# Optimization experiments

Hardware: AMD Instinct MI355X
Metric: run time of the kernel (lower is better)

Reference implementation:

```python
import jax, jax.numpy as jnp
import numpy as np

NUM_HEADS = 16
D_MODEL = 1024
D_K = D_MODEL // NUM_HEADS


def setup_inputs() -> dict:
    key = jax.random.key(0)
    ks = jax.random.split(key, 11)
    B, S, D = 1, 4096, D_MODEL
    scale = 1.0 / np.sqrt(D)
    return {
        "Q": jax.random.normal(ks[0], (B, S, D), jnp.float32),
        "K": jax.random.normal(ks[1], (B, S, D), jnp.float32),
        "V": jax.random.normal(ks[2], (B, S, D), jnp.float32),
        "W_Q": jax.random.normal(ks[3], (D, D), jnp.float32) * scale,
        "b_Q": jax.random.normal(ks[4], (D,), jnp.float32) * 0.02,
        "W_K": jax.random.normal(ks[5], (D, D), jnp.float32) * scale,
        "b_K": jax.random.normal(ks[6], (D,), jnp.float32) * 0.02,
        "W_V": jax.random.normal(ks[7], (D, D), jnp.float32) * scale,
        "b_V": jax.random.normal(ks[8], (D,), jnp.float32) * 0.02,
        "W_O": jax.random.normal(ks[9], (D, D), jnp.float32) * scale,
        "b_O": jax.random.normal(ks[10], (D,), jnp.float32) * 0.02,
    }


def _split_heads(x):
    # (B, S, D) -> (B, H, S, d_k)
    B, S, _ = x.shape
    return x.reshape(B, S, NUM_HEADS, D_K).transpose(0, 2, 1, 3)


def reference(Q, K, V, W_Q, b_Q, W_K, b_K, W_V, b_V, W_O, b_O):
    q = _split_heads(Q @ W_Q + b_Q)  # (B, H, S, d_k)
    k = _split_heads(K @ W_K + b_K)
    v = _split_heads(V @ W_V + b_V)
    inv_sqrt_dk = jnp.asarray(1.0 / np.sqrt(D_K), q.dtype)
    scores = jnp.einsum("bhqd,bhkd->bhqk", q, k) * inv_sqrt_dk  # (B, H, S, S)
    weights = jax.nn.softmax(scores, axis=-1)
    out = jnp.einsum("bhqk,bhkd->bhqd", weights, v)  # (B, H, S, d_k)
    B, _, S, _ = out.shape
    combined = out.transpose(0, 2, 1, 3).reshape(B, S, D_MODEL)
    return combined @ W_O + b_O
```

## Files before the change

kernel.cpp:

```cpp
#include <hip/hip_runtime.h>

typedef float f32x2 __attribute__((ext_vector_type(2)));
typedef float f32x4 __attribute__((ext_vector_type(4)));
typedef float f32x16 __attribute__((ext_vector_type(16)));
typedef short bf16x8 __attribute__((ext_vector_type(8)));
typedef unsigned u32x2 __attribute__((ext_vector_type(2)));
typedef unsigned short u16;

#define S_LEN 4096
#define DMODEL 1024
#define NH 16
#define DK 64

#define SCALE_Q 0.18033688f

static __device__ __forceinline__ u16 f2bf(float x) {
  union { float f; unsigned u; } v; v.f = x;
  unsigned r = v.u + 0x7fffu + ((v.u >> 16) & 1u);
  return (u16)(r >> 16);
}

static __device__ __forceinline__ float bf2f(u16 x) {
  union { unsigned u; float f; } v; v.u = ((unsigned)x) << 16;
  return v.f;
}

#if __has_builtin(__builtin_amdgcn_exp2f)
#define EXP2F __builtin_amdgcn_exp2f
#else
#define EXP2F exp2f
#endif

static __device__ __forceinline__ unsigned pkbf(float lo, float hi) {
  unsigned r;
  asm("v_cvt_pk_bf16_f32 %0, %1, %2" : "=v"(r) : "v"(lo), "v"(hi));
  return r;
}

static __device__ __forceinline__ void plswap(unsigned& a, unsigned& b, int hi) {
#if __has_builtin(__builtin_amdgcn_permlane32_swap)
  u32x2 r = __builtin_amdgcn_permlane32_swap(a, b, false, false);
  a = r.x; b = r.y;
  (void)hi;
#else
  unsigned ax = __shfl_xor(a, 32), bx = __shfl_xor(b, 32);
  unsigned na = hi ? bx : a;
  unsigned nb = hi ? b : ax;
  a = na; b = nb;
#endif
}

static __device__ __forceinline__ void gload16(const void* g, void* l) {
  void* gg = (void*)g;
  __builtin_amdgcn_global_load_lds(
      (__attribute__((address_space(1))) void*)gg,
      (__attribute__((address_space(3))) void*)l, 16, 0, 0);
}

__global__ __launch_bounds__(256) void wcast4(const float* __restrict__ W0,
                                              const float* __restrict__ W1,
                                              const float* __restrict__ W2,
                                              const float* __restrict__ W3,
                                              u16* __restrict__ Wt) {
  __shared__ float t[32][33];
  const int z = blockIdx.z;
  const float* W = (z == 0) ? W0 : (z == 1) ? W1 : (z == 2) ? W2 : W3;
  u16* dst = Wt + (size_t)z * DMODEL * DMODEL;
  const int x = threadIdx.x, y = threadIdx.y;
  const int n0 = blockIdx.x * 32, k0 = blockIdx.y * 32;
#pragma unroll
  for (int i = 0; i < 4; ++i)
    t[y + 8 * i][x] = W[(size_t)(k0 + y + 8 * i) * DMODEL + n0 + x];
  __syncthreads();
#pragma unroll
  for (int i = 0; i < 4; ++i)
    dst[(size_t)(n0 + y + 8 * i) * DMODEL + k0 + x] = f2bf(t[x][y + 8 * i]);
}

__global__ __launch_bounds__(256) void castbf3(const float* __restrict__ A,
                                               const float* __restrict__ B,
                                               const float* __restrict__ C,
                                               u16* __restrict__ out) {
  const int z = blockIdx.x >> 10;
  const int b = blockIdx.x & 1023;
  const float* src = (z == 0) ? A : (z == 1) ? B : C;
  u16* dst = out + (size_t)z * S_LEN * DMODEL;
  const int n8 = S_LEN * DMODEL / 8;
  for (int i = b * 256 + threadIdx.x; i < n8; i += 1024 * 256) {
    float4 a = ((const float4*)src)[2 * i];
    float4 c = ((const float4*)src)[2 * i + 1];
    union { ushort4 u[2]; int4 q; } t;
    t.u[0].x = f2bf(a.x); t.u[0].y = f2bf(a.y);
    t.u[0].z = f2bf(a.z); t.u[0].w = f2bf(a.w);
    t.u[1].x = f2bf(c.x); t.u[1].y = f2bf(c.y);
    t.u[1].z = f2bf(c.z); t.u[1].w = f2bf(c.w);
    ((int4*)dst)[i] = t.q;
  }
}

template <int MODE>
__global__ __launch_bounds__(256) void pgemm(const u16* __restrict__ Abase,
                                             const u16* __restrict__ Btbase,
                                             const float* __restrict__ bq,
                                             const float* __restrict__ bk,
                                             const float* __restrict__ bv,
                                             void* __restrict__ outbase) {
  __shared__ __align__(16) char Al[16384];
  __shared__ __align__(16) char Bl[16384];
  const int nblk = gridDim.x, cpx = nblk >> 3;
  const int b0 = blockIdx.x;
  const int bid = (b0 & 7) * cpx + (b0 >> 3);
  const int z = (MODE == 0) ? (bid >> 8) : 0;
  const int rem = bid & 255;
  const int nb = rem & 7, mb = rem >> 3;
  const int m0 = mb * 128, n0 = nb * 128;
  const int tid = threadIdx.x, lane = tid & 63, wid = tid >> 6;
  const int gq = lane >> 4, c16 = lane & 15;
  const int wm = (wid >> 1) * 64, wn = (wid & 1) * 64;
  const char* Ab = (const char*)(Abase + (size_t)z * S_LEN * DMODEL);
  const char* Bb = (const char*)(Btbase + (size_t)z * DMODEL * DMODEL);
  const float* bias = (z == 0) ? bq : (z == 1 ? bk : bv);
  const float scale = (MODE == 0 && z == 0) ? SCALE_Q : 1.0f;

  f32x4 acc[4][4] = {};

  for (int kt = 0; kt < 16; ++kt) {
    const int kb = kt * 128;
#pragma unroll
    for (int p = 0; p < 4; ++p) {
      int lin = p * 4096 + tid * 16;
      int row = lin >> 7;
      int colg = (lin & 127) ^ ((row & 7) << 4);
      gload16(Ab + (size_t)(m0 + row) * 2048 + kb + colg,
              Al + p * 4096 + wid * 1024);
    }
#pragma unroll
    for (int p = 0; p < 4; ++p) {
      int lin = p * 4096 + tid * 16;
      int row = lin >> 7;
      int colg = (lin & 127) ^ ((row & 7) << 4);
      gload16(Bb + (size_t)(n0 + row) * 2048 + kb + colg,
              Bl + p * 4096 + wid * 1024);
    }
    __syncthreads();
#pragma unroll
    for (int kk = 0; kk < 2; ++kk) {
      bf16x8 a[4], b[4];
#pragma unroll
      for (int m = 0; m < 4; ++m) {
        int row = wm + m * 16 + c16;
        a[m] = *(const bf16x8*)(Al + row * 128 +
                                ((kk * 64 + gq * 16) ^ ((row & 7) << 4)));
      }
#pragma unroll
      for (int n = 0; n < 4; ++n) {
        int row = wn + n * 16 + c16;
        b[n] = *(const bf16x8*)(Bl + row * 128 +
                                ((kk * 64 + gq * 16) ^ ((row & 7) << 4)));
      }
#pragma unroll
      for (int m = 0; m < 4; ++m)
#pragma unroll
        for (int n = 0; n < 4; ++n)
          acc[m][n] =
              __builtin_amdgcn_mfma_f32_16x16x32_bf16(a[m], b[n], acc[m][n], 0, 0, 0);
    }
    __syncthreads();
  }

#pragma unroll
  for (int m = 0; m < 4; ++m) {
#pragma unroll
    for (int n = 0; n < 4; ++n) {
      const int row = m0 + wm + m * 16 + gq * 4;
      const int col = n0 + wn + n * 16 + c16;
      const float bb = bias[col];
      if (MODE == 1) {
        float* of = (float*)outbase;
#pragma unroll
        for (int j = 0; j < 4; ++j)
          of[(size_t)(row + j) * DMODEL + col] = acc[m][n][j] + bb;
      } else if (z == 2) {
        u16* ov = (u16*)outbase + (size_t)2 * S_LEN * DMODEL;
        ushort4 u;
        u.x = f2bf(acc[m][n][0] + bb);
        u.y = f2bf(acc[m][n][1] + bb);
        u.z = f2bf(acc[m][n][2] + bb);
        u.w = f2bf(acc[m][n][3] + bb);
        *(ushort4*)(ov + ((size_t)(col >> 6) * DK + (col & 63)) * S_LEN + row) = u;
      } else {
        u16* oq = (u16*)outbase + (size_t)z * S_LEN * DMODEL;
#pragma unroll
        for (int j = 0; j < 4; ++j)
          oq[((size_t)(col >> 6) * S_LEN + row + j) * DK + (col & 63)] =
              f2bf((acc[m][n][j] + bb) * scale);
      }
    }
  }
}

__global__ __launch_bounds__(512) void attn2(const u16* __restrict__ q,
                                             const u16* __restrict__ k,
                                             const u16* __restrict__ vt,
                                             u16* __restrict__ Opart,
                                             float* __restrict__ Lpart) {
  __shared__ __align__(16) char smem[32768];
  const int bid0 = blockIdx.x;
  const int bid = (bid0 & 7) * 64 + (bid0 >> 3);
  const int h = bid >> 5;
  const int kvh = (bid >> 4) & 1;
  const int qblk = bid & 15;
  const int tid = threadIdx.x;
  const int wid = tid >> 6, lane = tid & 63;
  const int l31 = lane & 31, hi = lane >> 5;

  const char* kpb = (const char*)k + (size_t)h * S_LEN * (DK * 2);
  const char* vtb = (const char*)vt + (size_t)h * DK * (S_LEN * 2);

  const int q0w = qblk * 256 + wid * 32;
  const u16* qrow = q + ((size_t)h * S_LEN + q0w + l31) * DK;
  bf16x8 qf[4];
#pragma unroll
  for (int dt = 0; dt < 4; ++dt)
    qf[dt] = *(const bf16x8*)(qrow + dt * 16 + hi * 8);

  f32x16 o0 = {}, o1 = {};
  f32x2 lacc2 = {0.f, 0.f};

  const int woff = wid << 10;
  const int kt0 = kvh * 32;
  const int kt1 = kt0 + 32;

  const int swz = (l31 & 7) << 4;
  int dsa[4];
#pragma unroll
  for (int dt = 0; dt < 4; ++dt)
    dsa[dt] = (l31 << 7) + ((dt * 32 + hi * 16) ^ swz);

  const int lin = tid * 16;
  const int sw = lin ^ (((lin >> 7) & 7) << 4);
  const char* gk = kpb + (size_t)kt0 * 8192 + sw;
  const char* gv = vtb + (size_t)(lin >> 7) * 8192 + (size_t)kt0 * 128 + (sw & 127);

  gload16(gk, smem + woff);          gk += 8192;
  gload16(gv, smem + 8192 + woff);   gv += 128;

  auto body = [&](const int CUR, const int NXT, bool doStage) {
    if (doStage) {
      gload16(gk, smem + NXT + woff);          gk += 8192;
      gload16(gv, smem + NXT + 8192 + woff);   gv += 128;
      asm volatile("s_waitcnt vmcnt(2)" ::: "memory");
    } else {
      asm volatile("s_waitcnt vmcnt(0)" ::: "memory");
    }
    __builtin_amdgcn_s_barrier();

    const char* kb = smem + CUR;
    const char* vb = smem + CUR + 8192;

    f32x16 st0 = {}, st1 = {};
    __builtin_amdgcn_s_setprio(1);
#pragma unroll
    for (int dt = 0; dt < 4; ++dt) {
      bf16x8 k0 = *(const bf16x8*)(kb + dsa[dt]);
      bf16x8 k1 = *(const bf16x8*)(kb + 4096 + dsa[dt]);
      st0 = __builtin_amdgcn_mfma_f32_32x32x16_bf16(k0, qf[dt], st0, 0, 0, 0);
      st1 = __builtin_amdgcn_mfma_f32_32x32x16_bf16(k1, qf[dt], st1, 0, 0, 0);
    }
    __builtin_amdgcn_s_setprio(0);

    unsigned w0[8], w1[8];
    f32x2 s2 = {0.f, 0.f};
#pragma unroll
    for (int i = 0; i < 8; ++i) {
      float a0 = EXP2F(st0[2 * i]), a1 = EXP2F(st0[2 * i + 1]);
      f32x2 t = {a0, a1}; s2 += t;
      w0[i] = pkbf(a0, a1);
    }
#pragma unroll
    for (int i = 0; i < 8; ++i) {
      float a0 = EXP2F(st1[2 * i]), a1 = EXP2F(st1[2 * i + 1]);
      f32x2 t = {a0, a1}; s2 += t;
      w1[i] = pkbf(a0, a1);
    }
    lacc2 += s2;

    union UF { unsigned w[4]; bf16x8 v; };
    UF f[4];
#pragma unroll
    for (int g = 0; g < 2; ++g) {
#pragma unroll
      for (int j = 0; j < 2; ++j) {
        unsigned a = w0[4 * g + j], b = w0[4 * g + j + 2];
        plswap(a, b, hi);
        f[g].w[j] = a; f[g].w[j + 2] = b;
        unsigned c = w1[4 * g + j], d = w1[4 * g + j + 2];
        plswap(c, d, hi);
        f[2 + g].w[j] = c; f[2 + g].w[j + 2] = d;
      }
    }

    __builtin_amdgcn_s_setprio(1);
#pragma unroll
    for (int kt2 = 0; kt2 < 4; ++kt2) {
      bf16x8 v0 = *(const bf16x8*)(vb + dsa[kt2]);
      bf16x8 v1 = *(const bf16x8*)(vb + 4096 + dsa[kt2]);
      o0 = __builtin_amdgcn_mfma_f32_32x32x16_bf16(v0, f[kt2].v, o0, 0, 0, 0);
      o1 = __builtin_amdgcn_mfma_f32_32x32x16_bf16(v1, f[kt2].v, o1, 0, 0, 0);
    }
    __builtin_amdgcn_s_setprio(0);

    __builtin_amdgcn_s_barrier();
  };

  for (int kt = kt0; kt < kt1; kt += 2) {
    body(0, 16384, kt + 1 < kt1);
    body(16384, 0, kt + 2 < kt1);
  }

  const float lacc = lacc2.x + lacc2.y;
  const float lrow = lacc + __shfl_xor(lacc, 32);
  u16* Ob = Opart + ((((size_t)kvh * NH + h) * S_LEN) + q0w + l31) * DK;
#pragma unroll
  for (int g = 0; g < 4; ++g) {
    ushort4 u0, u1;
    u0.x = f2bf(o0[g * 4 + 0]); u0.y = f2bf(o0[g * 4 + 1]);
    u0.z = f2bf(o0[g * 4 + 2]); u0.w = f2bf(o0[g * 4 + 3]);
    *(ushort4*)(Ob + 8 * g + 4 * hi) = u0;
    u1.x = f2bf(o1[g * 4 + 0]); u1.y = f2bf(o1[g * 4 + 1]);
    u1.z = f2bf(o1[g * 4 + 2]); u1.w = f2bf(o1[g * 4 + 3]);
    *(ushort4*)(Ob + 32 + 8 * g + 4 * hi) = u1;
  }
  Lpart[((size_t)kvh * NH + h) * S_LEN + q0w + l31] = lrow;
}

__global__ __launch_bounds__(256) void combine(const u16* __restrict__ Op,
                                               const float* __restrict__ Lp,
                                               u16* __restrict__ comb) {
  const int id = blockIdx.x * 256 + threadIdx.x;
  const int h = id >> 16;
  const int rem = id & 65535;
  const int qv = rem >> 4;
  const int d4 = (rem & 15) << 2;
  const size_t str = (size_t)NH * S_LEN * DK;
  const size_t base = (((size_t)h * S_LEN) + qv) * DK + d4;
  float o0 = 0.f, o1 = 0.f, o2 = 0.f, o3 = 0.f, l = 0.f;
#pragma unroll
  for (int kv = 0; kv < 2; ++kv) {
    ushort4 u = *(const ushort4*)(Op + kv * str + base);
    o0 += bf2f(u.x); o1 += bf2f(u.y); o2 += bf2f(u.z); o3 += bf2f(u.w);
    l += Lp[(size_t)kv * NH * S_LEN + (size_t)h * S_LEN + qv];
  }
  const float inv = 1.f / l;
  ushort4 u;
  u.x = f2bf(o0 * inv);
  u.y = f2bf(o1 * inv);
  u.z = f2bf(o2 * inv);
  u.w = f2bf(o3 * inv);
  *(ushort4*)(comb + (size_t)qv * DMODEL + h * DK + d4) = u;
}

extern "C" void kernel_launch(void* const* d_in, const int* in_sizes, int n_in,
                              void* d_out, int out_size, void* d_ws, size_t ws_size,
                              hipStream_t stream) {
  (void)in_sizes; (void)n_in; (void)out_size; (void)ws_size;
  const float* Q   = (const float*)d_in[0];
  const float* K   = (const float*)d_in[1];
  const float* V   = (const float*)d_in[2];
  const float* W_Q = (const float*)d_in[3];
  const float* b_Q = (const float*)d_in[4];
  const float* W_K = (const float*)d_in[5];
  const float* b_K = (const float*)d_in[6];
  const float* W_V = (const float*)d_in[7];
  const float* b_V = (const float*)d_in[8];
  const float* W_O = (const float*)d_in[9];
  const float* b_O = (const float*)d_in[10];
  float* out = (float*)d_out;

  char* ws = (char*)d_ws;
  const size_t MB = 1024 * 1024;
  u16* WtQ = (u16*)ws;
  u16* Qbf = (u16*)(ws + 8 * MB);
  u16* Opart = (u16*)(ws + 8 * MB);
  u16* qp   = (u16*)(ws + 40 * MB);
  u16* kp   = qp + (size_t)S_LEN * DMODEL;
  u16* vtp  = kp + (size_t)S_LEN * DMODEL;
  u16* comb = vtp + (size_t)S_LEN * DMODEL;
  float* Lpart = (float*)(ws + 72 * MB);

  dim3 tb(32, 8);
  dim3 tg4(32, 32, 4);
  wcast4<<<tg4, tb, 0, stream>>>(W_Q, W_K, W_V, W_O, WtQ);

  castbf3<<<3072, 256, 0, stream>>>(Q, K, V, Qbf);

  pgemm<0><<<768, 256, 0, stream>>>(Qbf, WtQ, b_Q, b_K, b_V, qp);

  attn2<<<512, 512, 0, stream>>>(qp, kp, vtp, Opart, Lpart);
  combine<<<4096, 256, 0, stream>>>(Opart, Lpart, comb);

  pgemm<1><<<256, 256, 0, stream>>>(comb, WtQ + (size_t)3 * DMODEL * DMODEL,
                                    b_O, b_O, b_O, out);
}
```

Before: 168.7 us.

## Process two 32-row query tiles per wave in attention, halving block size

After: 188.7 us. 1.12x slower.

```diff
diff --git a/kernel.cpp b/kernel.cpp
--- a/kernel.cpp
+++ b/kernel.cpp
@@ -199,7 +199,7 @@
   }
 }
 
-__global__ __launch_bounds__(512) void attn2(const u16* __restrict__ q,
+__global__ __launch_bounds__(256) void attn2(const u16* __restrict__ q,
                                              const u16* __restrict__ k,
                                              const u16* __restrict__ vt,
                                              u16* __restrict__ Opart,
@@ -217,15 +217,18 @@
   const char* kpb = (const char*)k + (size_t)h * S_LEN * (DK * 2);
   const char* vtb = (const char*)vt + (size_t)h * DK * (S_LEN * 2);
 
-  const int q0w = qblk * 256 + wid * 32;
-  const u16* qrow = q + ((size_t)h * S_LEN + q0w + l31) * DK;
-  bf16x8 qf[4];
-#pragma unroll
-  for (int dt = 0; dt < 4; ++dt)
-    qf[dt] = *(const bf16x8*)(qrow + dt * 16 + hi * 8);
-
-  f32x16 o0 = {}, o1 = {};
-  f32x2 lacc2 = {0.f, 0.f};
+  const int q0w = qblk * 256 + wid * 64;
+  const u16* qrowA = q + ((size_t)h * S_LEN + q0w + l31) * DK;
+  const u16* qrowB = qrowA + 32 * DK;
+  bf16x8 qfA[4], qfB[4];
+#pragma unroll
+  for (int dt = 0; dt < 4; ++dt) {
+    qfA[dt] = *(const bf16x8*)(qrowA + dt * 16 + hi * 8);
+    qfB[dt] = *(const bf16x8*)(qrowB + dt * 16 + hi * 8);
+  }
+
+  f32x16 oA0 = {}, oA1 = {}, oB0 = {}, oB1 = {};
+  f32x2 laccA = {0.f, 0.f}, laccB = {0.f, 0.f};
 
   const int woff = wid << 10;
   const int kt0 = kvh * 32;
@@ -237,19 +240,26 @@
   for (int dt = 0; dt < 4; ++dt)
     dsa[dt] = (l31 << 7) + ((dt * 32 + hi * 16) ^ swz);
 
-  const int lin = tid * 16;
-  const int sw = lin ^ (((lin >> 7) & 7) << 4);
-  const char* gk = kpb + (size_t)kt0 * 8192 + sw;
-  const char* gv = vtb + (size_t)(lin >> 7) * 8192 + (size_t)kt0 * 128 + (sw & 127);
-
-  gload16(gk, smem + woff);          gk += 8192;
-  gload16(gv, smem + 8192 + woff);   gv += 128;
+  const int lin0 = tid * 16, lin1 = 4096 + tid * 16;
+  const int sw0 = lin0 ^ (((lin0 >> 7) & 7) << 4);
+  const int sw1 = lin1 ^ (((lin1 >> 7) & 7) << 4);
+  const char* gk0 = kpb + (size_t)kt0 * 8192 + sw0;
+  const char* gk1 = kpb + (size_t)kt0 * 8192 + sw1;
+  const char* gv0 = vtb + (size_t)(lin0 >> 7) * 8192 + (size_t)kt0 * 128 + (sw0 & 127);
+  const char* gv1 = vtb + (size_t)(lin1 >> 7) * 8192 + (size_t)kt0 * 128 + (sw1 & 127);
+
+  gload16(gk0, smem + woff);          gk0 += 8192;
+  gload16(gk1, smem + 4096 + woff);   gk1 += 8192;
+  gload16(gv0, smem + 8192 + woff);   gv0 += 128;
+  gload16(gv1, smem + 12288 + woff);  gv1 += 128;
 
   auto body = [&](const int CUR, const int NXT, bool doStage) {
     if (doStage) {
-      gload16(gk, smem + NXT + woff);          gk += 8192;
-      gload16(gv, smem + NXT + 8192 + woff);   gv += 128;
-      asm volatile("s_waitcnt vmcnt(2)" ::: "memory");
+      gload16(gk0, smem + NXT + woff);          gk0 += 8192;
+      gload16(gk1, smem + NXT + 4096 + woff);   gk1 += 8192;
+      gload16(gv0, smem + NXT + 8192 + woff);   gv0 += 128;
+      gload16(gv1, smem + NXT + 12288 + woff);  gv1 += 128;
+      asm volatile("s_waitcnt vmcnt(4)" ::: "memory");
     } else {
       asm volatile("s_waitcnt vmcnt(0)" ::: "memory");
     }
@@ -258,46 +268,77 @@
     const char* kb = smem + CUR;
     const char* vb = smem + CUR + 8192;
 
-    f32x16 st0 = {}, st1 = {};
+    f32x16 stA0 = {}, stA1 = {}, stB0 = {}, stB1 = {};
     __builtin_amdgcn_s_setprio(1);
 #pragma unroll
     for (int dt = 0; dt < 4; ++dt) {
       bf16x8 k0 = *(const bf16x8*)(kb + dsa[dt]);
       bf16x8 k1 = *(const bf16x8*)(kb + 4096 + dsa[dt]);
-      st0 = __builtin_amdgcn_mfma_f32_32x32x16_bf16(k0, qf[dt], st0, 0, 0, 0);
-      st1 = __builtin_amdgcn_mfma_f32_32x32x16_bf16(k1, qf[dt], st1, 0, 0, 0);
+      stA0 = __builtin_amdgcn_mfma_f32_32x32x16_bf16(k0, qfA[dt], stA0, 0, 0, 0);
+      stA1 = __builtin_amdgcn_mfma_f32_32x32x16_bf16(k1, qfA[dt], stA1, 0, 0, 0);
+      stB0 = __builtin_amdgcn_mfma_f32_32x32x16_bf16(k0, qfB[dt], stB0, 0, 0, 0);
+      stB1 = __builtin_amdgcn_mfma_f32_32x32x16_bf16(k1, qfB[dt], stB1, 0, 0, 0);
     }
     __builtin_amdgcn_s_setprio(0);
 
-    unsigned w0[8], w1[8];
-    f32x2 s2 = {0.f, 0.f};
-#pragma unroll
-    for (int i = 0; i < 8; ++i) {
-      float a0 = EXP2F(st0[2 * i]), a1 = EXP2F(st0[2 * i + 1]);
-      f32x2 t = {a0, a1}; s2 += t;
-      w0[i] = pkbf(a0, a1);
-    }
-#pragma unroll
-    for (int i = 0; i < 8; ++i) {
-      float a0 = EXP2F(st1[2 * i]), a1 = EXP2F(st1[2 * i + 1]);
-      f32x2 t = {a0, a1}; s2 += t;
-      w1[i] = pkbf(a0, a1);
-    }
-    lacc2 += s2;
-
     union UF { unsigned w[4]; bf16x8 v; };
-    UF f[4];
-#pragma unroll
-    for (int g = 0; g < 2; ++g) {
-#pragma unroll
-      for (int j = 0; j < 2; ++j) {
-        unsigned a = w0[4 * g + j], b = w0[4 * g + j + 2];
-        plswap(a, b, hi);
-        f[g].w[j] = a; f[g].w[j + 2] = b;
-        unsigned c = w1[4 * g + j], d = w1[4 * g + j + 2];
-        plswap(c, d, hi);
-        f[2 + g].w[j] = c; f[2 + g].w[j + 2] = d;
-      }
+    UF fA[4], fB[4];
+
+    {
+      unsigned w0[8], w1[8];
+      f32x2 s2 = {0.f, 0.f};
+#pragma unroll
+      for (int i = 0; i < 8; ++i) {
+        float a0 = EXP2F(stA0[2 * i]), a1 = EXP2F(stA0[2 * i + 1]);
+        f32x2 t = {a0, a1}; s2 += t;
+        w0[i] = pkbf(a0, a1);
+      }
+#pragma unroll
+      for (int i = 0; i < 8; ++i) {
+        float a0 = EXP2F(stA1[2 * i]), a1 = EXP2F(stA1[2 * i + 1]);
+        f32x2 t = {a0, a1}; s2 += t;
+        w1[i] = pkbf(a0, a1);
+      }
+      laccA += s2;
+#pragma unroll
+      for (int g = 0; g < 2; ++g)
+#pragma unroll
+        for (int j = 0; j < 2; ++j) {
+          unsigned a = w0[4 * g + j], b = w0[4 * g + j + 2];
+          plswap(a, b, hi);
+          fA[g].w[j] = a; fA[g].w[j + 2] = b;
+          unsigned c = w1[4 * g + j], d = w1[4 * g + j + 2];
+          plswap(c, d, hi);
+          fA[2 + g].w[j] = c; fA[2 + g].w[j + 2] = d;
+        }
+    }
+    {
+      unsigned w0[8], w1[8];
+      f32x2 s2 = {0.f, 0.f};
+#pragma unroll
+      for (int i = 0; i < 8; ++i) {
+        float a0 = EXP2F(stB0[2 * i]), a1 = EXP2F(stB0[2 * i + 1]);
+        f32x2 t = {a0, a1}; s2 += t;
+        w0[i] = pkbf(a0, a1);
+      }
+#pragma unroll
+      for (int i = 0; i < 8; ++i) {
+        float a0 = EXP2F(stB1[2 * i]), a1 = EXP2F(stB1[2 * i + 1]);
+        f32x2 t = {a0, a1}; s2 += t;
+        w1[i] = pkbf(a0, a1);
+      }
+      laccB += s2;
+#pragma unroll
+      for (int g = 0; g < 2; ++g)
+#pragma unroll
+        for (int j = 0; j < 2; ++j) {
+          unsigned a = w0[4 * g + j], b = w0[4 * g + j + 2];
+          plswap(a, b, hi);
+          fB[g].w[j] = a; fB[g].w[j + 2] = b;
+          unsigned c = w1[4 * g + j], d = w1[4 * g + j + 2];
+          plswap(c, d, hi);
+          fB[2 + g].w[j] = c; fB[2 + g].w[j + 2] = d;
+        }
     }
 
     __builtin_amdgcn_s_setprio(1);
@@ -305,8 +346,10 @@
     for (int kt2 = 0; kt2 < 4; ++kt2) {
       bf16x8 v0 = *(const bf16x8*)(vb + dsa[kt2]);
       bf16x8 v1 = *(const bf16x8*)(vb + 4096 + dsa[kt2]);
-      o0 = __builtin_amdgcn_mfma_f32_32x32x16_bf16(v0, f[kt2].v, o0, 0, 0, 0);
-      o1 = __builtin_amdgcn_mfma_f32_32x32x16_bf16(v1, f[kt2].v, o1, 0, 0, 0);
+      oA0 = __builtin_amdgcn_mfma_f32_32x32x16_bf16(v0, fA[kt2].v, oA0, 0, 0, 0);
+      oA1 = __builtin_amdgcn_mfma_f32_32x32x16_bf16(v1, fA[kt2].v, oA1, 0, 0, 0);
+      oB0 = __builtin_amdgcn_mfma_f32_32x32x16_bf16(v0, fB[kt2].v, oB0, 0, 0, 0);
+      oB1 = __builtin_amdgcn_mfma_f32_32x32x16_bf16(v1, fB[kt2].v, oB1, 0, 0, 0);
     }
     __builtin_amdgcn_s_setprio(0);
 
@@ -318,20 +361,30 @@
     body(16384, 0, kt + 2 < kt1);
   }
 
-  const float lacc = lacc2.x + lacc2.y;
-  const float lrow = lacc + __shfl_xor(lacc, 32);
-  u16* Ob = Opart + ((((size_t)kvh * NH + h) * S_LEN) + q0w + l31) * DK;
+  const float lA = laccA.x + laccA.y;
+  const float lrowA = lA + __shfl_xor(lA, 32);
+  const float lB = laccB.x + laccB.y;
+  const float lrowB = lB + __shfl_xor(lB, 32);
+  u16* ObA = Opart + ((((size_t)kvh * NH + h) * S_LEN) + q0w + l31) * DK;
+  u16* ObB = ObA + (size_t)32 * DK;
 #pragma unroll
   for (int g = 0; g < 4; ++g) {
-    ushort4 u0, u1;
-    u0.x = f2bf(o0[g * 4 + 0]); u0.y = f2bf(o0[g * 4 + 1]);
-    u0.z = f2bf(o0[g * 4 + 2]); u0.w = f2bf(o0[g * 4 + 3]);
-    *(ushort4*)(Ob + 8 * g + 4 * hi) = u0;
-    u1.x = f2bf(o1[g * 4 + 0]); u1.y = f2bf(o1[g * 4 + 1]);
-    u1.z = f2bf(o1[g * 4 + 2]); u1.w = f2bf(o1[g * 4 + 3]);
-    *(ushort4*)(Ob + 32 + 8 * g + 4 * hi) = u1;
-  }
-  Lpart[((size_t)kvh * NH + h) * S_LEN + q0w + l31] = lrow;
+    ushort4 u;
+    u.x = f2bf(oA0[g * 4 + 0]); u.y = f2bf(oA0[g * 4 + 1]);
+    u.z = f2bf(oA0[g * 4 + 2]); u.w = f2bf(oA0[g * 4 + 3]);
+    *(ushort4*)(ObA + 8 * g + 4 * hi) = u;
+    u.x = f2bf(oA1[g * 4 + 0]); u.y = f2bf(oA1[g * 4 + 1]);
+    u.z = f2bf(oA1[g * 4 + 2]); u.w = f2bf(oA1[g * 4 + 3]);
+    *(ushort4*)(ObA + 32 + 8 * g + 4 * hi) = u;
+    u.x = f2bf(oB0[g * 4 + 0]); u.y = f2bf(oB0[g * 4 + 1]);
+    u.z = f2bf(oB0[g * 4 + 2]); u.w = f2bf(oB0[g * 4 + 3]);
+    *(ushort4*)(ObB + 8 * g + 4 * hi) = u;
+    u.x = f2bf(oB1[g * 4 + 0]); u.y = f2bf(oB1[g * 4 + 1]);
+    u.z = f2bf(oB1[g * 4 + 2]); u.w = f2bf(oB1[g * 4 + 3]);
+    *(ushort4*)(ObB + 32 + 8 * g + 4 * hi) = u;
+  }
+  Lpart[((size_t)kvh * NH + h) * S_LEN + q0w + l31] = lrowA;
+  Lpart[((size_t)kvh * NH + h) * S_LEN + q0w + 32 + l31] = lrowB;
 }
 
 __global__ __launch_bounds__(256) void combine(const u16* __restrict__ Op,
@@ -396,7 +449,7 @@
 
   pgemm<0><<<768, 256, 0, stream>>>(Qbf, WtQ, b_Q, b_K, b_V, qp);
 
-  attn2<<<512, 512, 0, stream>>>(qp, kp, vtp, Opart, Lpart);
+  attn2<<<512, 256, 0, stream>>>(qp, kp, vtp, Opart, Lpart);
   combine<<<4096, 256, 0, stream>>>(Opart, Lpart, comb);
 
   pgemm<1><<<256, 256, 0, stream>>>(comb, WtQ + (size_t)3 * DMODEL * DMODEL,
```

## Software-pipeline attention: overlap PV of previous tile with QK of current, 4-stage buffers

Applied to the files above, without the earlier changes.

Result: no change. 171.1 us (+1.4%).

```diff
diff --git a/kernel.cpp b/kernel.cpp
--- a/kernel.cpp
+++ b/kernel.cpp
@@ -199,12 +199,12 @@
   }
 }
 
-__global__ __launch_bounds__(512) void attn2(const u16* __restrict__ q,
-                                             const u16* __restrict__ k,
-                                             const u16* __restrict__ vt,
-                                             u16* __restrict__ Opart,
-                                             float* __restrict__ Lpart) {
-  __shared__ __align__(16) char smem[32768];
+__global__ __launch_bounds__(512, 4) void attn2(const u16* __restrict__ q,
+                                                const u16* __restrict__ k,
+                                                const u16* __restrict__ vt,
+                                                u16* __restrict__ Opart,
+                                                float* __restrict__ Lpart) {
+  __shared__ __align__(16) char smem[65536];
   const int bid0 = blockIdx.x;
   const int bid = (bid0 & 7) * 64 + (bid0 >> 3);
   const int h = bid >> 5;
@@ -229,7 +229,6 @@
 
   const int woff = wid << 10;
   const int kt0 = kvh * 32;
-  const int kt1 = kt0 + 32;
 
   const int swz = (l31 & 7) << 4;
   int dsa[4];
@@ -242,22 +241,15 @@
   const char* gk = kpb + (size_t)kt0 * 8192 + sw;
   const char* gv = vtb + (size_t)(lin >> 7) * 8192 + (size_t)kt0 * 128 + (sw & 127);
 
-  gload16(gk, smem + woff);          gk += 8192;
-  gload16(gv, smem + 8192 + woff);   gv += 128;
-
-  auto body = [&](const int CUR, const int NXT, bool doStage) {
-    if (doStage) {
-      gload16(gk, smem + NXT + woff);          gk += 8192;
-      gload16(gv, smem + NXT + 8192 + woff);   gv += 128;
-      asm volatile("s_waitcnt vmcnt(2)" ::: "memory");
-    } else {
-      asm volatile("s_waitcnt vmcnt(0)" ::: "memory");
-    }
-    __builtin_amdgcn_s_barrier();
-
-    const char* kb = smem + CUR;
-    const char* vb = smem + CUR + 8192;
-
+  gload16(gk, smem + woff);                  gk += 8192;
+  gload16(gv, smem + 8192 + woff);           gv += 128;
+  gload16(gk, smem + 16384 + woff);          gk += 8192;
+  gload16(gv, smem + 16384 + 8192 + woff);   gv += 128;
+
+  union UF { unsigned w[4]; bf16x8 v; };
+  UF fprev[4];
+
+  auto phase = [&](const char* kb, const char* vb, bool dopv) {
     f32x16 st0 = {}, st1 = {};
     __builtin_amdgcn_s_setprio(1);
 #pragma unroll
@@ -266,6 +258,12 @@
       bf16x8 k1 = *(const bf16x8*)(kb + 4096 + dsa[dt]);
       st0 = __builtin_amdgcn_mfma_f32_32x32x16_bf16(k0, qf[dt], st0, 0, 0, 0);
       st1 = __builtin_amdgcn_mfma_f32_32x32x16_bf16(k1, qf[dt], st1, 0, 0, 0);
+      if (dopv) {
+        bf16x8 v0 = *(const bf16x8*)(vb + dsa[dt]);
+        bf16x8 v1 = *(const bf16x8*)(vb + 4096 + dsa[dt]);
+        o0 = __builtin_amdgcn_mfma_f32_32x32x16_bf16(v0, fprev[dt].v, o0, 0, 0, 0);
+        o1 = __builtin_amdgcn_mfma_f32_32x32x16_bf16(v1, fprev[dt].v, o1, 0, 0, 0);
+      }
     }
     __builtin_amdgcn_s_setprio(0);
 
@@ -274,48 +272,71 @@
 #pragma unroll
     for (int i = 0; i < 8; ++i) {
       float a0 = EXP2F(st0[2 * i]), a1 = EXP2F(st0[2 * i + 1]);
-      f32x2 t = {a0, a1}; s2 += t;
+      f32x2 tt = {a0, a1}; s2 += tt;
       w0[i] = pkbf(a0, a1);
     }
 #pragma unroll
     for (int i = 0; i < 8; ++i) {
       float a0 = EXP2F(st1[2 * i]), a1 = EXP2F(st1[2 * i + 1]);
-      f32x2 t = {a0, a1}; s2 += t;
+      f32x2 tt = {a0, a1}; s2 += tt;
       w1[i] = pkbf(a0, a1);
     }
     lacc2 += s2;
-
-    union UF { unsigned w[4]; bf16x8 v; };
-    UF f[4];
-#pragma unroll
-    for (int g = 0; g < 2; ++g) {
+#pragma unroll
+    for (int g = 0; g < 2; ++g)
 #pragma unroll
       for (int j = 0; j < 2; ++j) {
         unsigned a = w0[4 * g + j], b = w0[4 * g + j + 2];
         plswap(a, b, hi);
-        f[g].w[j] = a; f[g].w[j + 2] = b;
+        fprev[g].w[j] = a; fprev[g].w[j + 2] = b;
         unsigned c = w1[4 * g + j], d = w1[4 * g + j + 2];
         plswap(c, d, hi);
-        f[2 + g].w[j] = c; f[2 + g].w[j + 2] = d;
+        fprev[2 + g].w[j] = c; fprev[2 + g].w[j + 2] = d;
       }
-    }
-
+  };
+
+  __builtin_amdgcn_sched_barrier(0);
+  gload16(gk, smem + 32768 + woff);         gk += 8192;
+  gload16(gv, smem + 32768 + 8192 + woff);  gv += 128;
+  asm volatile("s_waitcnt vmcnt(4)" ::: "memory");
+  __builtin_amdgcn_s_barrier();
+  phase(smem, smem, false);
+  __builtin_amdgcn_s_barrier();
+
+  for (int t = 1; t <= 29; ++t) {
+    __builtin_amdgcn_sched_barrier(0);
+    const int bs = ((t + 2) & 3) << 14;
+    gload16(gk, smem + bs + woff);         gk += 8192;
+    gload16(gv, smem + bs + 8192 + woff);  gv += 128;
+    asm volatile("s_waitcnt vmcnt(4)" ::: "memory");
+    __builtin_amdgcn_s_barrier();
+    phase(smem + ((t & 3) << 14), smem + (((t + 3) & 3) << 14) + 8192, true);
+    __builtin_amdgcn_s_barrier();
+  }
+
+  __builtin_amdgcn_sched_barrier(0);
+  asm volatile("s_waitcnt vmcnt(2)" ::: "memory");
+  __builtin_amdgcn_s_barrier();
+  phase(smem + ((30 & 3) << 14), smem + ((29 & 3) << 14) + 8192, true);
+  __builtin_amdgcn_s_barrier();
+
+  __builtin_amdgcn_sched_barrier(0);
+  asm volatile("s_waitcnt vmcnt(0)" ::: "memory");
+  __builtin_amdgcn_s_barrier();
+  phase(smem + ((31 & 3) << 14), smem + ((30 & 3) << 14) + 8192, true);
+  __builtin_amdgcn_s_barrier();
+
+  {
+    const char* vb = smem + ((31 & 3) << 14) + 8192;
     __builtin_amdgcn_s_setprio(1);
 #pragma unroll
-    for (int kt2 = 0; kt2 < 4; ++kt2) {
-      bf16x8 v0 = *(const bf16x8*)(vb + dsa[kt2]);
-      bf16x8 v1 = *(const bf16x8*)(vb + 4096 + dsa[kt2]);
-      o0 = __builtin_amdgcn_mfma_f32_32x32x16_bf16(v0, f[kt2].v, o0, 0, 0, 0);
-      o1 = __builtin_amdgcn_mfma_f32_32x32x16_bf16(v1, f[kt2].v, o1, 0, 0, 0);
+    for (int dt = 0; dt < 4; ++dt) {
+      bf16x8 v0 = *(const bf16x8*)(vb + dsa[dt]);
+      bf16x8 v1 = *(const bf16x8*)(vb + 4096 + dsa[dt]);
+      o0 = __builtin_amdgcn_mfma_f32_32x32x16_bf16(v0, fprev[dt].v, o0, 0, 0, 0);
+      o1 = __builtin_amdgcn_mfma_f32_32x32x16_bf16(v1, fprev[dt].v, o1, 0, 0, 0);
     }
     __builtin_amdgcn_s_setprio(0);
-
-    __builtin_amdgcn_s_barrier();
-  };
-
-  for (int kt = kt0; kt < kt1; kt += 2) {
-    body(0, 16384, kt + 1 < kt1);
-    body(16384, 0, kt + 2 < kt1);
   }
 
   const float lacc = lacc2.x + lacc2.y;
```
